# Performance work log

Measured on AMD Instinct MI355X. Metric: run time of the kernel, lower is better.

## Reference

```python
import jax, jax.numpy as jnp
import numpy as np

N = 50000
E = 800000
DIM_IN = 128
DIM_H = 16
HEADS = 8
DIM_OUT = 16
NEG_SLOPE = 0.2


def setup_inputs() -> dict:
    key = jax.random.key(0)
    ks = jax.random.split(key, 12)
    def glorot(k, shape):
        fan_in = shape[0]
        return jax.random.normal(k, shape, dtype=jnp.float32) / np.sqrt(fan_in)
    x = jax.random.normal(ks[0], (N, DIM_IN), dtype=jnp.float32)
    edge_index = jax.random.randint(ks[1], (2, E), 0, N, dtype=jnp.int64)
    # layer 1: GATv2Conv(dim_in, dim_h, heads=8)
    Wl1 = glorot(ks[2], (DIM_IN, HEADS * DIM_H))
    Wr1 = glorot(ks[3], (DIM_IN, HEADS * DIM_H))
    att1 = glorot(ks[4], (HEADS, DIM_H))
    bias1 = jnp.zeros((HEADS * DIM_H,), dtype=jnp.float32)
    # layer 2: GATv2Conv(dim_h*heads, dim_out, heads=1)
    Wl2 = glorot(ks[5], (HEADS * DIM_H, DIM_OUT))
    Wr2 = glorot(ks[6], (HEADS * DIM_H, DIM_OUT))
    att2 = glorot(ks[7], (1, DIM_OUT))
    bias2 = jnp.zeros((DIM_OUT,), dtype=jnp.float32)
    return {"x": x, "edge_index": edge_index, "Wl1": Wl1, "Wr1": Wr1,
            "att1": att1, "bias1": bias1, "Wl2": Wl2, "Wr2": Wr2,
            "att2": att2, "bias2": bias2}


def gatv2_layer(x, src, dst, Wl, Wr, att, bias, n_nodes, heads, ch):
    # x: [N, F_in]; src/dst: [Etot] (self-loops included)
    xl = (x @ Wl).reshape(n_nodes, heads, ch)  # source transform
    xr = (x @ Wr).reshape(n_nodes, heads, ch)  # target transform
    e = jax.nn.leaky_relu(xl[src] + xr[dst], NEG_SLOPE)      # [Etot, H, C]
    logits = jnp.einsum('ehc,hc->eh', e, att)                # [Etot, H]
    # segment softmax over incoming edges of each target node
    m = jax.ops.segment_max(logits, dst, num_segments=n_nodes)
    a = jnp.exp(logits - m[dst])
    denom = jax.ops.segment_sum(a, dst, num_segments=n_nodes)
    alpha = a / denom[dst]                                   # [Etot, H]
    out = jax.ops.segment_sum(xl[src] * alpha[:, :, None], dst,
                              num_segments=n_nodes)          # [N, H, C]
    return out.reshape(n_nodes, heads * ch) + bias


def reference(x, edge_index, Wl1, Wr1, att1, bias1, Wl2, Wr2, att2, bias2):
    # PyG GATv2Conv adds self-loops by default
    loops = jnp.arange(N, dtype=edge_index.dtype)
    src = jnp.concatenate([edge_index[0], loops])
    dst = jnp.concatenate([edge_index[1], loops])
    # dropout is identity in eval mode
    h = gatv2_layer(x, src, dst, Wl1, Wr1, att1, bias1, N, HEADS, DIM_H)
    h = jax.nn.elu(h)
    h = gatv2_layer(h, src, dst, Wl2, Wr2, att2, bias2, N, 1, DIM_OUT)
    return h, jax.nn.log_softmax(h, axis=1)
```

## Files before the change

### kernel.cpp

```cpp
#include <hip/hip_runtime.h>
#include <hip/hip_bf16.h>
#include <hip/hip_fp16.h>
#include <math.h>

#define NN 50000
#define EE 800000
#define DIN 128
#define HEADS 8
#define DH 16
#define DOUT 16
#define NEG 0.2f
#define GM 32
#define GB ((NN + GM - 1) / GM)
#define NB ((NN + 255) / 256)
#define ABLK ((EE / 4 + 255) / 256)
#define NPART 8
#define RANGE (NN / NPART)
#define RB 1563
#define SCATB 64
#define BUCKCAP 110000
#define PAD 64

typedef __attribute__((ext_vector_type(8))) short bf16x8;
typedef __attribute__((ext_vector_type(4))) float f32x4;
typedef __attribute__((ext_vector_type(4))) int i32x4;

__device__ __forceinline__ unsigned pack2bf(float a, float b) {
    union { __hip_bfloat162 h; unsigned u; } c;
    c.h = __float22bfloat162_rn(make_float2(a, b));
    return c.u;
}
__device__ __forceinline__ unsigned short f2bf(float v) {
    union { __hip_bfloat16 h; unsigned short u; } c;
    c.h = __float2bfloat16(v);
    return c.u;
}
__device__ __forceinline__ unsigned short f2h(float v) {
    union { __half h; unsigned short u; } c;
    c.h = __float2half(v);
    return c.u;
}
__device__ __forceinline__ float bflo(unsigned u) { return __uint_as_float(u << 16); }
__device__ __forceinline__ float bfhi(unsigned u) { return __uint_as_float(u & 0xffff0000u); }
__device__ __forceinline__ float h2lo(unsigned u) {
    union { unsigned short s; __half h; } c; c.s = (unsigned short)(u & 0xffffu);
    return __half2float(c.h);
}
__device__ __forceinline__ float h2hi(unsigned u) {
    union { unsigned short s; __half h; } c; c.s = (unsigned short)(u >> 16);
    return __half2float(c.h);
}
__device__ __forceinline__ float elu1(float x) { return x > 0.f ? x : __expf(x) - 1.f; }

__global__ __launch_bounds__(256) void init_bucket(int* __restrict__ cnt,
                                                   const float* __restrict__ Wl,
                                                   const float* __restrict__ Wr,
                                                   unsigned short* __restrict__ Wb,
                                                   const float* __restrict__ Wl2,
                                                   const float* __restrict__ Wr2,
                                                   unsigned short* __restrict__ Wb2,
                                                   const int* __restrict__ ei,
                                                   unsigned* __restrict__ bhead,
                                                   unsigned* __restrict__ bucket) {
    int b = blockIdx.x, t = threadIdx.x;
    if (b < NB) {
        int i = b * 256 + t;
        if (i < NN) cnt[i] = 1;
        return;
    } else if (b < NB + 128) {
        int i = (b - NB) * 256 + t;
        int n = i >> 7, k = i & 127;
        float v = (n < 128) ? Wl[k * 128 + n] : Wr[k * 128 + (n - 128)];
        Wb[i] = f2bf(v);
        return;
    } else if (b < NB + 144) {
        int i = (b - NB - 128) * 256 + t;
        int n = i >> 7, k = i & 127;
        float v = (n < 16) ? Wl2[k * 16 + n] : Wr2[k * 16 + (n - 16)];
        Wb2[i] = f2bf(v);
        return;
    }
    __shared__ unsigned lrec[1024];
    __shared__ unsigned lcnt[8], loff[8], lpos[8], gbase[8];
    int ab = b - (NB + 144);
    int i = ab * 256 + t;
    bool valid = i < EE / 4;
    i32x4 ss, dd;
    unsigned bb[4];
    if (valid) {
        ss = __builtin_nontemporal_load(((const i32x4*)ei) + i);
        dd = __builtin_nontemporal_load(((const i32x4*)(ei + EE)) + i);
    }
    if (t < 8) { lcnt[t] = 0; lpos[t] = 0; }
    __syncthreads();
    if (valid) {
#pragma unroll
        for (int e = 0; e < 4; ++e) {
            bb[e] = (unsigned)dd[e] / RANGE;
            atomicAdd(&lcnt[bb[e]], 1u);
        }
    }
    __syncthreads();
    if (t == 0) {
        unsigned run = 0;
#pragma unroll
        for (int q = 0; q < 8; ++q) { loff[q] = run; run += lcnt[q]; }
    }
    if (t < 8 && lcnt[t] > 0) gbase[t] = atomicAdd(&bhead[t], lcnt[t]);
    __syncthreads();
    if (valid) {
#pragma unroll
        for (int e = 0; e < 4; ++e) {
            unsigned p = atomicAdd(&lpos[bb[e]], 1u);
            lrec[loff[bb[e]] + p] = ((unsigned)ss[e] << 16) | (unsigned)dd[e];
        }
    }
    __syncthreads();
    unsigned total = loff[7] + lcnt[7];
    for (unsigned j = t; j < total; j += 256) {
        unsigned q = 0;
        while (q < 7 && j >= loff[q + 1]) ++q;
        bucket[(size_t)q * BUCKCAP + gbase[q] + (j - loff[q])] = lrec[j];
    }
}

__global__ __launch_bounds__(256) void scat_gemm1(const unsigned* __restrict__ bucket,
                                                  const unsigned* __restrict__ bhead,
                                                  int* __restrict__ cnt,
                                                  unsigned short* __restrict__ esrcPad,
                                                  const float* __restrict__ x,
                                                  const unsigned short* __restrict__ Wb,
                                                  unsigned short* __restrict__ xlb,
                                                  unsigned short* __restrict__ xr) {
    __shared__ unsigned short As[GM][136];
    __shared__ unsigned short Cs[GM][264];
    int t = threadIdx.x;
    if (blockIdx.x < NPART * SCATB) {
        int r = blockIdx.x & 7;
        int g = blockIdx.x >> 3;
        if (g == 0) {
            for (int dq = t; dq < RANGE; dq += 256) {
                int d = r * RANGE + dq;
                esrcPad[(unsigned)d * PAD] = (unsigned short)d;
            }
        }
        unsigned n = bhead[r];
        for (unsigned i = (unsigned)g * 256 + t; i < n; i += SCATB * 256) {
            unsigned rec = __builtin_nontemporal_load(bucket + (size_t)r * BUCKCAP + i);
            unsigned s = rec >> 16, d = rec & 0xffffu;
            int p = atomicAdd(&cnt[d], 1);
            esrcPad[d * PAD + p] = (unsigned short)s;
        }
        return;
    }
    int n0 = (blockIdx.x - NPART * SCATB) * GM;
    {
        int row = t >> 3, seg = t & 7;
        int nsrc = n0 + row < NN ? n0 + row : NN - 1;
        const f32x4* xp = (const f32x4*)(x + (size_t)nsrc * DIN + 16 * seg);
        f32x4 v0 = __builtin_nontemporal_load(xp);
        f32x4 v1 = __builtin_nontemporal_load(xp + 1);
        f32x4 v2 = __builtin_nontemporal_load(xp + 2);
        f32x4 v3 = __builtin_nontemporal_load(xp + 3);
        uint4 p0 = make_uint4(pack2bf(v0[0], v0[1]), pack2bf(v0[2], v0[3]),
                              pack2bf(v1[0], v1[1]), pack2bf(v1[2], v1[3]));
        uint4 p1 = make_uint4(pack2bf(v2[0], v2[1]), pack2bf(v2[2], v2[3]),
                              pack2bf(v3[0], v3[1]), pack2bf(v3[2], v3[3]));
        *(uint4*)&As[row][16 * seg]     = p0;
        *(uint4*)&As[row][16 * seg + 8] = p1;
    }
    __syncthreads();
    int lane = t & 63, w = t >> 6;
    int m = lane & 15, quad = lane >> 4;
    f32x4 acc[2][4];
#pragma unroll
    for (int mt = 0; mt < 2; ++mt)
#pragma unroll
        for (int nt = 0; nt < 4; ++nt) acc[mt][nt] = (f32x4){0.f, 0.f, 0.f, 0.f};
#pragma unroll
    for (int ks = 0; ks < 4; ++ks) {
        int k = 32 * ks + 8 * quad;
        bf16x8 a0 = *(const bf16x8*)&As[m][k];
        bf16x8 a1 = *(const bf16x8*)&As[16 + m][k];
#pragma unroll
        for (int nt = 0; nt < 4; ++nt) {
            int n = 64 * w + 16 * nt + m;
            bf16x8 b = *(const bf16x8*)(Wb + (size_t)n * 128 + k);
            acc[0][nt] = __builtin_amdgcn_mfma_f32_16x16x32_bf16(a0, b, acc[0][nt], 0, 0, 0);
            acc[1][nt] = __builtin_amdgcn_mfma_f32_16x16x32_bf16(a1, b, acc[1][nt], 0, 0, 0);
        }
    }
#pragma unroll
    for (int mt = 0; mt < 2; ++mt) {
#pragma unroll
        for (int nt = 0; nt < 4; ++nt) {
            int col = 64 * w + 16 * nt + m;
            int rbase = 16 * mt + 4 * quad;
            if (col < 128) {
#pragma unroll
                for (int r = 0; r < 4; ++r) Cs[rbase + r][col] = f2bf(acc[mt][nt][r]);
            } else {
#pragma unroll
                for (int r = 0; r < 4; ++r) Cs[rbase + r][col] = f2h(acc[mt][nt][r]);
            }
        }
    }
    __syncthreads();
    {
        int row = t >> 3, seg = t & 7;
        int grow = n0 + row;
        if (grow < NN) {
            uint4 a0 = *(uint4*)&Cs[row][16 * seg];
            uint4 a1 = *(uint4*)&Cs[row][16 * seg + 8];
            *(uint4*)(xlb + (unsigned)grow * DIN + 16 * seg)     = a0;
            *(uint4*)(xlb + (unsigned)grow * DIN + 16 * seg + 8) = a1;
            uint4 b0 = *(uint4*)&Cs[row][128 + 16 * seg];
            uint4 b1 = *(uint4*)&Cs[row][128 + 16 * seg + 8];
            *(uint4*)(xr + (unsigned)grow * DIN + 16 * seg)     = b0;
            *(uint4*)(xr + (unsigned)grow * DIN + 16 * seg + 8) = b1;
        }
    }
}

__global__ __launch_bounds__(256) void l1_fused(const unsigned short* __restrict__ esrcPad,
                                                const int* __restrict__ cnt,
                                                const unsigned short* __restrict__ xlb,
                                                const unsigned short* __restrict__ xr,
                                                const float* __restrict__ att,
                                                const float* __restrict__ bias,
                                                unsigned short* __restrict__ hb) {
    int r = blockIdx.x & 7;
    int dq = (blockIdx.x >> 3) * 4 + (threadIdx.x >> 6);
    if (dq >= RANGE) return;
    int d = r * RANGE + dq;
    int lane = threadIdx.x & 63;
    int quarter = lane >> 4;
    int q16 = lane & 15;
    int rs = d * PAD;
    int re = rs + cnt[d];
    int last = re - 1;
    uint4 xru = ((const uint4*)(xr + (unsigned)d * DIN))[q16];
    float4 xr0, xr1;
    xr0.x = h2lo(xru.x); xr0.y = h2hi(xru.x);
    xr0.z = h2lo(xru.y); xr0.w = h2hi(xru.y);
    xr1.x = h2lo(xru.z); xr1.y = h2hi(xru.z);
    xr1.z = h2lo(xru.w); xr1.w = h2hi(xru.w);
    float4 at0 = ((const float4*)att)[2 * q16];
    float4 at1 = ((const float4*)att)[2 * q16 + 1];
    float4 a0 = make_float4(0.f, 0.f, 0.f, 0.f);
    float4 a1 = make_float4(0.f, 0.f, 0.f, 0.f);
    float l = 0.f;
    int slot = rs + quarter;
    int c0 = slot < last ? slot : last;
    unsigned s0 = esrcPad[c0];
    int c1 = slot + 4 < last ? slot + 4 : last;
    unsigned s1 = esrcPad[c1];
    uint4 row = ((const uint4*)(xlb + s0 * (unsigned)DIN))[q16];
    for (; slot < re; slot += 4) {
        uint4 cur = row;
        int c2 = slot + 8 < last ? slot + 8 : last;
        unsigned s2 = esrcPad[c2];
        row = ((const uint4*)(xlb + s1 * (unsigned)DIN))[q16];
        s1 = s2;
        float f0 = bflo(cur.x), f1 = bfhi(cur.x);
        float f2 = bflo(cur.y), f3 = bfhi(cur.y);
        float f4 = bflo(cur.z), f5 = bfhi(cur.z);
        float f6 = bflo(cur.w), f7 = bfhi(cur.w);
        float v0 = f0 + xr0.x; v0 = fmaxf(v0, NEG * v0);
        float v1 = f1 + xr0.y; v1 = fmaxf(v1, NEG * v1);
        float v2 = f2 + xr0.z; v2 = fmaxf(v2, NEG * v2);
        float v3 = f3 + xr0.w; v3 = fmaxf(v3, NEG * v3);
        float v4 = f4 + xr1.x; v4 = fmaxf(v4, NEG * v4);
        float v5 = f5 + xr1.y; v5 = fmaxf(v5, NEG * v5);
        float v6 = f6 + xr1.z; v6 = fmaxf(v6, NEG * v6);
        float v7 = f7 + xr1.w; v7 = fmaxf(v7, NEG * v7);
        float w = at0.x * v0 + at0.y * v1 + at0.z * v2 + at0.w * v3
                + at1.x * v4 + at1.y * v5 + at1.z * v6 + at1.w * v7;
        w += __shfl_xor(w, 1);
        float p = __expf(w);
        a0.x += p * f0; a0.y += p * f1; a0.z += p * f2; a0.w += p * f3;
        a1.x += p * f4; a1.y += p * f5; a1.z += p * f6; a1.w += p * f7;
        l += p;
    }
#pragma unroll
    for (int off = 16; off < 64; off <<= 1) {
        a0.x += __shfl_xor(a0.x, off); a0.y += __shfl_xor(a0.y, off);
        a0.z += __shfl_xor(a0.z, off); a0.w += __shfl_xor(a0.w, off);
        a1.x += __shfl_xor(a1.x, off); a1.y += __shfl_xor(a1.y, off);
        a1.z += __shfl_xor(a1.z, off); a1.w += __shfl_xor(a1.w, off);
        l += __shfl_xor(l, off);
    }
    if (quarter == 0) {
        float inv = 1.f / l;
        float4 b0 = ((const float4*)bias)[2 * q16];
        float4 b1 = ((const float4*)bias)[2 * q16 + 1];
        float4 o0, o1;
        o0.x = elu1(a0.x * inv + b0.x);
        o0.y = elu1(a0.y * inv + b0.y);
        o0.z = elu1(a0.z * inv + b0.z);
        o0.w = elu1(a0.w * inv + b0.w);
        o1.x = elu1(a1.x * inv + b1.x);
        o1.y = elu1(a1.y * inv + b1.y);
        o1.z = elu1(a1.z * inv + b1.z);
        o1.w = elu1(a1.w * inv + b1.w);
        uint4 pk = make_uint4(pack2bf(o0.x, o0.y), pack2bf(o0.z, o0.w),
                              pack2bf(o1.x, o1.y), pack2bf(o1.z, o1.w));
        ((uint4*)(hb + (unsigned)d * DIN))[q16] = pk;
    }
}

__global__ __launch_bounds__(256) void gemm2(const unsigned short* __restrict__ hb,
                                             const unsigned short* __restrict__ Wb2,
                                             float* __restrict__ xl2, float* __restrict__ xr2) {
    __shared__ unsigned short As[GM][136];
    int t = threadIdx.x;
    int n0 = blockIdx.x * GM;
    {
        int row = t >> 3, s8 = t & 7;
        int nsrc = n0 + row < NN ? n0 + row : NN - 1;
        const uint4* src = (const uint4*)(hb + (size_t)nsrc * DIN);
        *(uint4*)&As[row][8 * s8]      = src[s8];
        *(uint4*)&As[row][8 * s8 + 64] = src[s8 + 8];
    }
    __syncthreads();
    int lane = t & 63, w = t >> 6;
    int m = lane & 15, quad = lane >> 4;
    int mt = w & 1, nt = w >> 1;
    f32x4 acc = (f32x4){0.f, 0.f, 0.f, 0.f};
#pragma unroll
    for (int ks = 0; ks < 4; ++ks) {
        int k = 32 * ks + 8 * quad;
        bf16x8 a = *(const bf16x8*)&As[16 * mt + m][k];
        bf16x8 b = *(const bf16x8*)(Wb2 + (size_t)(16 * nt + m) * 128 + k);
        acc = __builtin_amdgcn_mfma_f32_16x16x32_bf16(a, b, acc, 0, 0, 0);
    }
    float* __restrict__ dst = (nt == 0) ? xl2 : xr2;
#pragma unroll
    for (int r = 0; r < 4; ++r) {
        int node = n0 + 16 * mt + 4 * quad + r;
        if (node < NN) dst[(size_t)node * DOUT + m] = acc[r];
    }
}

__global__ __launch_bounds__(256) void l2_fused(const unsigned short* __restrict__ esrcPad,
                                                const int* __restrict__ cnt,
                                                const float* __restrict__ xl,
                                                const float* __restrict__ xr,
                                                const float* __restrict__ att,
                                                const float* __restrict__ bias,
                                                float* __restrict__ out) {
    int r = blockIdx.x & 7;
    int dq = (blockIdx.x >> 3) * 4 + (threadIdx.x >> 6);
    if (dq >= RANGE) return;
    int d = r * RANGE + dq;
    int lane = threadIdx.x & 63;
    int sl = lane >> 2;
    int q = lane & 3;
    int rs = d * PAD;
    int re = rs + cnt[d];
    int last = re - 1;
    float4 xrq = ((const float4*)(xr + (unsigned)d * DOUT))[q];
    float4 atq = ((const float4*)att)[q];
    float4 acc = make_float4(0.f, 0.f, 0.f, 0.f);
    float l = 0.f;
    int slot = rs + sl;
    int c0 = slot < last ? slot : last;
    unsigned s0 = esrcPad[c0];
    for (; slot < re; slot += 16) {
        int c1 = slot + 16 < last ? slot + 16 : last;
        unsigned s1 = esrcPad[c1];
        float4 cur = ((const float4*)(xl + s0 * (unsigned)DOUT))[q];
        s0 = s1;
        float v0 = cur.x + xrq.x; v0 = fmaxf(v0, NEG * v0);
        float v1 = cur.y + xrq.y; v1 = fmaxf(v1, NEG * v1);
        float v2 = cur.z + xrq.z; v2 = fmaxf(v2, NEG * v2);
        float v3 = cur.w + xrq.w; v3 = fmaxf(v3, NEG * v3);
        float w = atq.x * v0 + atq.y * v1 + atq.z * v2 + atq.w * v3;
        w += __shfl_xor(w, 1);
        w += __shfl_xor(w, 2);
        float p = __expf(w);
        acc.x += p * cur.x; acc.y += p * cur.y;
        acc.z += p * cur.z; acc.w += p * cur.w;
        l += p;
    }
#pragma unroll
    for (int off = 4; off < 64; off <<= 1) {
        acc.x += __shfl_xor(acc.x, off);
        acc.y += __shfl_xor(acc.y, off);
        acc.z += __shfl_xor(acc.z, off);
        acc.w += __shfl_xor(acc.w, off);
        l += __shfl_xor(l, off);
    }
    float inv = 1.f / l;
    float4 b = ((const float4*)bias)[q];
    float4 v;
    v.x = acc.x * inv + b.x; v.y = acc.y * inv + b.y;
    v.z = acc.z * inv + b.z; v.w = acc.w * inv + b.w;
    float m = fmaxf(fmaxf(v.x, v.y), fmaxf(v.z, v.w));
    m = fmaxf(m, __shfl_xor(m, 1));
    m = fmaxf(m, __shfl_xor(m, 2));
    float es = __expf(v.x - m) + __expf(v.y - m) + __expf(v.z - m) + __expf(v.w - m);
    es += __shfl_xor(es, 1);
    es += __shfl_xor(es, 2);
    float lse = m + __logf(es);
    if (sl == 0) {
        ((float4*)(out + (size_t)d * DOUT))[q] = v;
        float4 ls;
        ls.x = v.x - lse; ls.y = v.y - lse; ls.z = v.z - lse; ls.w = v.w - lse;
        ((float4*)(out + (size_t)NN * DOUT + (size_t)d * DOUT))[q] = ls;
    }
}

extern "C" void kernel_launch(void* const* d_in, const int* in_sizes, int n_in,
                              void* d_out, int out_size, void* d_ws, size_t ws_size,
                              hipStream_t stream) {
    const float* x     = (const float*)d_in[0];
    const int*   ei    = (const int*)d_in[1];
    const float* Wl1   = (const float*)d_in[2];
    const float* Wr1   = (const float*)d_in[3];
    const float* att1  = (const float*)d_in[4];
    const float* bias1 = (const float*)d_in[5];
    const float* Wl2   = (const float*)d_in[6];
    const float* Wr2   = (const float*)d_in[7];
    const float* att2  = (const float*)d_in[8];
    const float* bias2 = (const float*)d_in[9];
    float* out = (float*)d_out;

    unsigned short* xr1 = (unsigned short*)d_ws;
    float* xl2    = (float*)(xr1 + (size_t)NN * DIN);
    float* xr2    = xl2 + (size_t)NN * DOUT;
    unsigned short* xlb = (unsigned short*)(xr2 + (size_t)NN * DOUT);
    unsigned short* hb  = xlb + (size_t)NN * DIN;
    unsigned short* Wb  = hb + (size_t)NN * DIN;
    unsigned short* Wb2 = Wb + 256 * 128;
    unsigned short* esrcPad = Wb2 + 32 * 128;
    int*   cnt    = (int*)(esrcPad + (size_t)NN * PAD);
    unsigned* bucket = (unsigned*)(cnt + NN);
    unsigned* bhead  = bucket + (size_t)8 * BUCKCAP;

    const int B = 256;
    hipMemsetAsync(bhead, 0, 8 * sizeof(unsigned), stream);
    init_bucket<<<NB + 144 + ABLK, B, 0, stream>>>(cnt, Wl1, Wr1, Wb, Wl2, Wr2, Wb2,
                                                   ei, bhead, bucket);
    scat_gemm1<<<NPART * SCATB + GB, B, 0, stream>>>(bucket, bhead, cnt, esrcPad,
                                                     x, Wb, xlb, xr1);
    l1_fused<<<NPART * RB, B, 0, stream>>>(esrcPad, cnt, xlb, xr1, att1, bias1, hb);
    gemm2<<<GB, B, 0, stream>>>(hb, Wb2, xl2, xr2);
    l2_fused<<<NPART * RB, B, 0, stream>>>(esrcPad, cnt, xl2, xr2, att2, bias2, out);
}
```

Baseline: 227.7 us.

## Regroup preprocessing kernels so edge bucketing overlaps the first GEMM

The weight conversion moves into its own small kernel. Edge bucketing and counter init are co-scheduled with the layer-1 GEMM blocks in one launch, and the bucket-to-CSR scatter becomes a separate kernel after it. The bucketing pass reuses the GEMM's shared-memory arrays. The goal is to run the bandwidth-bound edge partitioning concurrently with the GEMM rather than the atomic scatter. The cost is one extra kernel launch and a different mix of co-resident blocks.

```diff
diff --git a/kernel.cpp b/kernel.cpp
--- a/kernel.cpp
+++ b/kernel.cpp
@@ -52,108 +52,91 @@
 }
 __device__ __forceinline__ float elu1(float x) { return x > 0.f ? x : __expf(x) - 1.f; }
 
-__global__ __launch_bounds__(256) void init_bucket(int* __restrict__ cnt,
-                                                   const float* __restrict__ Wl,
-                                                   const float* __restrict__ Wr,
-                                                   unsigned short* __restrict__ Wb,
-                                                   const float* __restrict__ Wl2,
-                                                   const float* __restrict__ Wr2,
-                                                   unsigned short* __restrict__ Wb2,
-                                                   const int* __restrict__ ei,
-                                                   unsigned* __restrict__ bhead,
-                                                   unsigned* __restrict__ bucket) {
+__global__ __launch_bounds__(256) void wcvt(const float* __restrict__ Wl,
+                                            const float* __restrict__ Wr,
+                                            unsigned short* __restrict__ Wb,
+                                            const float* __restrict__ Wl2,
+                                            const float* __restrict__ Wr2,
+                                            unsigned short* __restrict__ Wb2) {
     int b = blockIdx.x, t = threadIdx.x;
-    if (b < NB) {
+    if (b < 128) {
         int i = b * 256 + t;
-        if (i < NN) cnt[i] = 1;
-        return;
-    } else if (b < NB + 128) {
-        int i = (b - NB) * 256 + t;
         int n = i >> 7, k = i & 127;
         float v = (n < 128) ? Wl[k * 128 + n] : Wr[k * 128 + (n - 128)];
         Wb[i] = f2bf(v);
-        return;
-    } else if (b < NB + 144) {
-        int i = (b - NB - 128) * 256 + t;
+    } else {
+        int i = (b - 128) * 256 + t;
         int n = i >> 7, k = i & 127;
         float v = (n < 16) ? Wl2[k * 16 + n] : Wr2[k * 16 + (n - 16)];
         Wb2[i] = f2bf(v);
-        return;
-    }
-    __shared__ unsigned lrec[1024];
-    __shared__ unsigned lcnt[8], loff[8], lpos[8], gbase[8];
-    int ab = b - (NB + 144);
-    int i = ab * 256 + t;
-    bool valid = i < EE / 4;
-    i32x4 ss, dd;
-    unsigned bb[4];
-    if (valid) {
-        ss = __builtin_nontemporal_load(((const i32x4*)ei) + i);
-        dd = __builtin_nontemporal_load(((const i32x4*)(ei + EE)) + i);
-    }
-    if (t < 8) { lcnt[t] = 0; lpos[t] = 0; }
-    __syncthreads();
-    if (valid) {
-#pragma unroll
-        for (int e = 0; e < 4; ++e) {
-            bb[e] = (unsigned)dd[e] / RANGE;
-            atomicAdd(&lcnt[bb[e]], 1u);
-        }
-    }
-    __syncthreads();
-    if (t == 0) {
-        unsigned run = 0;
-#pragma unroll
-        for (int q = 0; q < 8; ++q) { loff[q] = run; run += lcnt[q]; }
-    }
-    if (t < 8 && lcnt[t] > 0) gbase[t] = atomicAdd(&bhead[t], lcnt[t]);
-    __syncthreads();
-    if (valid) {
-#pragma unroll
-        for (int e = 0; e < 4; ++e) {
-            unsigned p = atomicAdd(&lpos[bb[e]], 1u);
-            lrec[loff[bb[e]] + p] = ((unsigned)ss[e] << 16) | (unsigned)dd[e];
-        }
-    }
-    __syncthreads();
-    unsigned total = loff[7] + lcnt[7];
-    for (unsigned j = t; j < total; j += 256) {
-        unsigned q = 0;
-        while (q < 7 && j >= loff[q + 1]) ++q;
-        bucket[(size_t)q * BUCKCAP + gbase[q] + (j - loff[q])] = lrec[j];
-    }
-}
-
-__global__ __launch_bounds__(256) void scat_gemm1(const unsigned* __restrict__ bucket,
-                                                  const unsigned* __restrict__ bhead,
-                                                  int* __restrict__ cnt,
-                                                  unsigned short* __restrict__ esrcPad,
-                                                  const float* __restrict__ x,
-                                                  const unsigned short* __restrict__ Wb,
-                                                  unsigned short* __restrict__ xlb,
-                                                  unsigned short* __restrict__ xr) {
+    }
+}
+
+__global__ __launch_bounds__(256) void bucket_gemm1(int* __restrict__ cnt,
+                                                    const int* __restrict__ ei,
+                                                    unsigned* __restrict__ bhead,
+                                                    unsigned* __restrict__ bucket,
+                                                    const float* __restrict__ x,
+                                                    const unsigned short* __restrict__ Wb,
+                                                    unsigned short* __restrict__ xlb,
+                                                    unsigned short* __restrict__ xr) {
     __shared__ unsigned short As[GM][136];
     __shared__ unsigned short Cs[GM][264];
     int t = threadIdx.x;
-    if (blockIdx.x < NPART * SCATB) {
-        int r = blockIdx.x & 7;
-        int g = blockIdx.x >> 3;
-        if (g == 0) {
-            for (int dq = t; dq < RANGE; dq += 256) {
-                int d = r * RANGE + dq;
-                esrcPad[(unsigned)d * PAD] = (unsigned short)d;
+    if (blockIdx.x < NB) {
+        int i = blockIdx.x * 256 + t;
+        if (i < NN) cnt[i] = 1;
+        return;
+    }
+    if (blockIdx.x < NB + ABLK) {
+        unsigned* lrec = (unsigned*)&As[0][0];
+        unsigned* lcnt = (unsigned*)&Cs[0][0];
+        unsigned* loff = lcnt + 8;
+        unsigned* lpos = loff + 8;
+        unsigned* gbase = lpos + 8;
+        int ab = blockIdx.x - NB;
+        int i = ab * 256 + t;
+        bool valid = i < EE / 4;
+        i32x4 ss, dd;
+        unsigned bb[4];
+        if (valid) {
+            ss = __builtin_nontemporal_load(((const i32x4*)ei) + i);
+            dd = __builtin_nontemporal_load(((const i32x4*)(ei + EE)) + i);
+        }
+        if (t < 8) { lcnt[t] = 0; lpos[t] = 0; }
+        __syncthreads();
+        if (valid) {
+#pragma unroll
+            for (int e = 0; e < 4; ++e) {
+                bb[e] = (unsigned)dd[e] / RANGE;
+                atomicAdd(&lcnt[bb[e]], 1u);
             }
         }
-        unsigned n = bhead[r];
-        for (unsigned i = (unsigned)g * 256 + t; i < n; i += SCATB * 256) {
-            unsigned rec = __builtin_nontemporal_load(bucket + (size_t)r * BUCKCAP + i);
-            unsigned s = rec >> 16, d = rec & 0xffffu;
-            int p = atomicAdd(&cnt[d], 1);
-            esrcPad[d * PAD + p] = (unsigned short)s;
+        __syncthreads();
+        if (t == 0) {
+            unsigned run = 0;
+#pragma unroll
+            for (int q = 0; q < 8; ++q) { loff[q] = run; run += lcnt[q]; }
+        }
+        if (t < 8 && lcnt[t] > 0) gbase[t] = atomicAdd(&bhead[t], lcnt[t]);
+        __syncthreads();
+        if (valid) {
+#pragma unroll
+            for (int e = 0; e < 4; ++e) {
+                unsigned p = atomicAdd(&lpos[bb[e]], 1u);
+                lrec[loff[bb[e]] + p] = ((unsigned)ss[e] << 16) | (unsigned)dd[e];
+            }
+        }
+        __syncthreads();
+        unsigned total = loff[7] + lcnt[7];
+        for (unsigned j = t; j < total; j += 256) {
+            unsigned q = 0;
+            while (q < 7 && j >= loff[q + 1]) ++q;
+            bucket[(size_t)q * BUCKCAP + gbase[q] + (j - loff[q])] = lrec[j];
         }
         return;
     }
-    int n0 = (blockIdx.x - NPART * SCATB) * GM;
+    int n0 = (blockIdx.x - (NB + ABLK)) * GM;
     {
         int row = t >> 3, seg = t & 7;
         int nsrc = n0 + row < NN ? n0 + row : NN - 1;
@@ -219,6 +202,28 @@
             *(uint4*)(xr + (unsigned)grow * DIN + 16 * seg)     = b0;
             *(uint4*)(xr + (unsigned)grow * DIN + 16 * seg + 8) = b1;
         }
+    }
+}
+
+__global__ __launch_bounds__(256) void scatter_b(const unsigned* __restrict__ bucket,
+                                                 const unsigned* __restrict__ bhead,
+                                                 int* __restrict__ cnt,
+                                                 unsigned short* __restrict__ esrcPad) {
+    int r = blockIdx.x & 7;
+    int g = blockIdx.x >> 3;
+    int t = threadIdx.x;
+    if (g == 0) {
+        for (int dq = t; dq < RANGE; dq += 256) {
+            int d = r * RANGE + dq;
+            esrcPad[(unsigned)d * PAD] = (unsigned short)d;
+        }
+    }
+    unsigned n = bhead[r];
+    for (unsigned i = (unsigned)g * 256 + t; i < n; i += SCATB * 256) {
+        unsigned rec = __builtin_nontemporal_load(bucket + (size_t)r * BUCKCAP + i);
+        unsigned s = rec >> 16, d = rec & 0xffffu;
+        int p = atomicAdd(&cnt[d], 1);
+        esrcPad[d * PAD + p] = (unsigned short)s;
     }
 }
 
@@ -440,10 +445,10 @@
 
     const int B = 256;
     hipMemsetAsync(bhead, 0, 8 * sizeof(unsigned), stream);
-    init_bucket<<<NB + 144 + ABLK, B, 0, stream>>>(cnt, Wl1, Wr1, Wb, Wl2, Wr2, Wb2,
-                                                   ei, bhead, bucket);
-    scat_gemm1<<<NPART * SCATB + GB, B, 0, stream>>>(bucket, bhead, cnt, esrcPad,
-                                                     x, Wb, xlb, xr1);
+    wcvt<<<144, B, 0, stream>>>(Wl1, Wr1, Wb, Wl2, Wr2, Wb2);
+    bucket_gemm1<<<NB + ABLK + GB, B, 0, stream>>>(cnt, ei, bhead, bucket,
+                                                   x, Wb, xlb, xr1);
+    scatter_b<<<NPART * SCATB, B, 0, stream>>>(bucket, bhead, cnt, esrcPad);
     l1_fused<<<NPART * RB, B, 0, stream>>>(esrcPad, cnt, xlb, xr1, att1, bias1, hb);
     gemm2<<<GB, B, 0, stream>>>(hb, Wb2, xl2, xr2);
     l2_fused<<<NPART * RB, B, 0, stream>>>(esrcPad, cnt, xl2, xr2, att2, bias2, out);
```

Result: slower. 236.3 us (+3.8%).
